# Kernel tuning notes

Hardware: AMD Instinct MI355X
Metric: run time of the kernel (lower is better)

The kernel has to match this reference:

```python
import jax, jax.numpy as jnp
import numpy as np

OUT_H, OUT_W = 14, 14
SPATIAL_SCALE = 0.25

def setup_inputs() -> dict:
    key = jax.random.key(0)
    k1, k2, k3, k4, k5, k6 = jax.random.split(key, 6)
    B, C, H, W = 2, 256, 200, 336
    R = 1000
    features = jax.random.normal(k1, (B, C, H, W), jnp.float32)
    img_h, img_w = H / SPATIAL_SCALE, W / SPATIAL_SCALE
    cx = jax.random.uniform(k2, (R,)) * img_w
    cy = jax.random.uniform(k3, (R,)) * img_h
    bw = jax.random.uniform(k4, (R,)) * 256.0 + 16.0
    bh = jax.random.uniform(k5, (R,)) * 256.0 + 16.0
    x1 = jnp.clip(cx - bw / 2, 0.0, img_w - 1.0)
    x2 = jnp.clip(cx + bw / 2, 0.0, img_w - 1.0)
    y1 = jnp.clip(cy - bh / 2, 0.0, img_h - 1.0)
    y2 = jnp.clip(cy + bh / 2, 0.0, img_h - 1.0)
    bidx = jax.random.randint(k6, (R,), 0, B).astype(jnp.float32)
    rois = jnp.stack([bidx, x1, y1, x2, y2], axis=1)  # (R, 5)
    return {"features": features, "rois": rois}

def _roi_align(features, rois):
    # features: (B, C, H, W); rois: (R, 5) = (batch_idx, x1, y1, x2, y2) in image coords
    B, C, H, W = features.shape
    R = rois.shape[0]
    b = jax.lax.stop_gradient(rois[:, 0]).astype(jnp.int32)
    x1, y1, x2, y2 = rois[:, 1], rois[:, 2], rois[:, 3], rois[:, 4]
    # bin-center grid in [0,1] (affine_grid identity, align_corners=False, then normalized)
    gx = (jnp.arange(OUT_W, dtype=features.dtype) + 0.5) / OUT_W
    gy = (jnp.arange(OUT_H, dtype=features.dtype) + 0.5) / OUT_H
    px = x1[:, None] + gx[None, :] * (x2 - x1)[:, None]  # (R, OUT_W) abs image x
    py = y1[:, None] + gy[None, :] * (y2 - y1)[:, None]  # (R, OUT_H) abs image y
    # grid_sample(align_corners=False) with normalized coord abs/(size/scale): pix = abs*scale - 0.5
    fx = jnp.broadcast_to(px[:, None, :], (R, OUT_H, OUT_W)) * SPATIAL_SCALE - 0.5
    fy = jnp.broadcast_to(py[:, :, None], (R, OUT_H, OUT_W)) * SPATIAL_SCALE - 0.5
    x0 = jnp.floor(fx); y0 = jnp.floor(fy)
    lx = fx - x0; ly = fy - y0
    x0i = x0.astype(jnp.int32); y0i = y0.astype(jnp.int32)
    feats_flat = features.reshape(B, C, H * W)
    bb = b[:, None, None]  # (R,1,1)
    def corner(yi, xi):
        valid = ((xi >= 0) & (xi < W) & (yi >= 0) & (yi < H)).astype(features.dtype)
        idx = jnp.clip(yi, 0, H - 1) * W + jnp.clip(xi, 0, W - 1)  # (R,OUT_H,OUT_W)
        v = feats_flat[bb, :, idx]  # (R, OUT_H, OUT_W, C)
        return v * valid[..., None]  # zeros padding_mode
    v00 = corner(y0i, x0i)
    v01 = corner(y0i, x0i + 1)
    v10 = corner(y0i + 1, x0i)
    v11 = corner(y0i + 1, x0i + 1)
    wx0 = (1.0 - lx)[..., None]; wx1 = lx[..., None]
    wy0 = (1.0 - ly)[..., None]; wy1 = ly[..., None]
    out = wy0 * (wx0 * v00 + wx1 * v01) + wy1 * (wx0 * v10 + wx1 * v11)
    return out.transpose(0, 3, 1, 2)  # (R, C, OUT_H, OUT_W)

def reference(features, rois):
    return _roi_align(features, rois)
```

## Files before the change

### kernel.cpp

```cpp
#include <hip/hip_runtime.h>

constexpr int B = 2, C = 256, H = 200, W = 336;
constexpr int HW = H * W;
constexpr int OH = 14, OW = 14, OHW = OH * OW;
constexpr float SCALE = 0.25f;
constexpr int R = 1000;

constexpr int CSPLIT = 4;
constexpr int CPB = C / CSPLIT;
constexpr int NXCD = 8;
constexpr int RPX = R / NXCD;

typedef float f2 __attribute__((ext_vector_type(2), aligned(4)));

__global__ __launch_bounds__(1024) void sort_rois_kernel(
    const float* __restrict__ rois, int* __restrict__ order)
{
    __shared__ unsigned key[1024];
    const int t = threadIdx.x;

    unsigned k = 0xFFFFFFFFu;
    if (t < R) {
        const float* roi = rois + t * 5;
        const int   b  = (int)roi[0];
        const float cx = 0.5f * (roi[1] + roi[3]);
        const float cy = 0.5f * (roi[2] + roi[4]);
        const int yb   = min(12, max(0, (int)cy >> 6));
        const int band = (b << 4) | yb;
        const int cxi  = min(2047, max(0, (int)cx));
        k = ((unsigned)band << 21) | ((unsigned)cxi << 10) | (unsigned)t;
    }
    key[t] = k;

    for (int size = 2; size <= 1024; size <<= 1) {
        for (int stride = size >> 1; stride > 0; stride >>= 1) {
            __syncthreads();
            const int j = t ^ stride;
            if (j > t) {
                const bool up = ((t & size) == 0);
                const unsigned a = key[t], b2 = key[j];
                if ((a > b2) == up) { key[t] = b2; key[j] = a; }
            }
        }
    }
    __syncthreads();
    if (t < R) order[t] = (int)(key[t] & 1023u);
}

__global__ __launch_bounds__(256) void roi_align_kernel(
    const float* __restrict__ feat,
    const float* __restrict__ rois,
    const int*  __restrict__ order,
    float* __restrict__ out)
{
    const int bid   = blockIdx.x;
    const int xcd   = bid & (NXCD - 1);
    const int slot  = bid >> 3;
    const int slice = slot & (CSPLIT - 1);
    const int rank  = slot >> 2;
    const int r     = order[xcd * RPX + rank];
    const int c0    = slice * CPB;
    const int tid   = threadIdx.x;

    const float* roi = rois + r * 5;
    const float bf = roi[0];
    const float x1 = roi[1], y1 = roi[2], x2 = roi[3], y2 = roi[4];
    const int b = __builtin_amdgcn_readfirstlane((int)bf);

    const int s = tid;
    if (s >= OHW) return;

    const int oh = s / OW;
    const int ow = s - oh * OW;

    const float fx = (x1 + (ow + 0.5f) * (1.0f / OW) * (x2 - x1)) * SCALE - 0.5f;
    const float fy = (y1 + (oh + 0.5f) * (1.0f / OH) * (y2 - y1)) * SCALE - 0.5f;

    const float x0f = floorf(fx), y0f = floorf(fy);
    const float lx = fx - x0f,   ly = fy - y0f;
    const int x0 = (int)x0f,  y0 = (int)y0f;
    const int x1i = x0 + 1,   y1i = y0 + 1;

    const float cxw0 = ((x0  >= 0 && x0  < W) ? 1.0f : 0.0f) * (1.0f - lx);
    const float cxw1 = ((x1i >= 0 && x1i < W) ? 1.0f : 0.0f) * lx;
    const float ryw0 = ((y0  >= 0 && y0  < H) ? 1.0f : 0.0f) * (1.0f - ly);
    const float ryw1 = ((y1i >= 0 && y1i < H) ? 1.0f : 0.0f) * ly;

    const int px = min(max(x0, 0), W - 2);
    const bool swp = (x0 != px);
    const float wxa = swp ? cxw1 : cxw0;
    const float wxb = swp ? cxw0 : cxw1;
    const float a0 = ryw0 * wxa, b0 = ryw0 * wxb;
    const float a1 = ryw1 * wxa, b1 = ryw1 * wxb;

    const int cy0 = min(max(y0,  0), H - 1);
    const int cy1 = min(max(y1i, 0), H - 1);
    const int i0 = cy0 * W + px;
    const int i1 = cy1 * W + px;

    const float* p  = feat + (size_t)(b * C + c0) * HW;
    float*       op = out  + (size_t)r * C * OHW + (size_t)c0 * OHW + s;

    #pragma unroll 8
    for (int c = 0; c < CPB; ++c) {
        const f2 r0 = *reinterpret_cast<const f2*>(p + i0);
        const f2 r1 = *reinterpret_cast<const f2*>(p + i1);
        *op = fmaf(a0, r0.x, fmaf(b0, r0.y, fmaf(a1, r1.x, b1 * r1.y)));
        p  += HW;
        op += OHW;
    }
}

extern "C" void kernel_launch(void* const* d_in, const int* in_sizes, int n_in,
                              void* d_out, int out_size, void* d_ws, size_t ws_size,
                              hipStream_t stream) {
    const float* feat = (const float*)d_in[0];
    const float* rois = (const float*)d_in[1];
    float* out = (float*)d_out;
    int* order = (int*)d_ws;

    sort_rois_kernel<<<1, 1024, 0, stream>>>(rois, order);

    dim3 grid(R * CSPLIT);
    dim3 block(256);
    roi_align_kernel<<<grid, block, 0, stream>>>(feat, rois, order, out);
}
```

Baseline: 413.3 us.

## Bucket ROIs by 2D tile, split channels 16 ways, batch loads, nontemporal stores

Replaces the bitonic sort of ROIs with a counting-sort over batch/y/x tiles of 64 pixels, using shared-memory atomics and a prefix scan. This gives 2D locality instead of row-band ordering, though ROIs within a bucket end up in nondeterministic order. The channel split rises from 4 to 16, so there are four times as many smaller blocks, and launch bounds request higher occupancy. The inner loop now issues 8 channels of gathers before computing, and writes output with nontemporal stores to avoid polluting cache.

After: 387.4 us. -6.3%, faster.

```diff
diff --git a/kernel.cpp b/kernel.cpp
--- a/kernel.cpp
+++ b/kernel.cpp
@@ -6,48 +6,52 @@
 constexpr float SCALE = 0.25f;
 constexpr int R = 1000;
 
-constexpr int CSPLIT = 4;
+constexpr int CSPLIT = 16;
 constexpr int CPB = C / CSPLIT;
 constexpr int NXCD = 8;
 constexpr int RPX = R / NXCD;
 
+constexpr int NYB = 13;
+constexpr int NXB = 21;
+constexpr int NBUCKET = B * NYB * NXB;
+
 typedef float f2 __attribute__((ext_vector_type(2), aligned(4)));
 
-__global__ __launch_bounds__(1024) void sort_rois_kernel(
+__global__ __launch_bounds__(1024) void bucket_rois_kernel(
     const float* __restrict__ rois, int* __restrict__ order)
 {
-    __shared__ unsigned key[1024];
+    __shared__ int cnt[1024];
     const int t = threadIdx.x;
+    cnt[t] = 0;
+    __syncthreads();
 
-    unsigned k = 0xFFFFFFFFu;
+    int k = 0, pos = 0;
     if (t < R) {
         const float* roi = rois + t * 5;
         const int   b  = (int)roi[0];
         const float cx = 0.5f * (roi[1] + roi[3]);
         const float cy = 0.5f * (roi[2] + roi[4]);
-        const int yb   = min(12, max(0, (int)cy >> 6));
-        const int band = (b << 4) | yb;
-        const int cxi  = min(2047, max(0, (int)cx));
-        k = ((unsigned)band << 21) | ((unsigned)cxi << 10) | (unsigned)t;
-    }
-    key[t] = k;
-
-    for (int size = 2; size <= 1024; size <<= 1) {
-        for (int stride = size >> 1; stride > 0; stride >>= 1) {
-            __syncthreads();
-            const int j = t ^ stride;
-            if (j > t) {
-                const bool up = ((t & size) == 0);
-                const unsigned a = key[t], b2 = key[j];
-                if ((a > b2) == up) { key[t] = b2; key[j] = a; }
-            }
-        }
+        const int yb = min(NYB - 1, max(0, (int)cy >> 6));
+        const int xb = min(NXB - 1, max(0, (int)cx >> 6));
+        k = (b * NYB + yb) * NXB + xb;
+        pos = atomicAdd(&cnt[k], 1);
     }
     __syncthreads();
-    if (t < R) order[t] = (int)(key[t] & 1023u);
+
+    for (int off = 1; off < 1024; off <<= 1) {
+        const int add = (t >= off) ? cnt[t - off] : 0;
+        __syncthreads();
+        cnt[t] += add;
+        __syncthreads();
+    }
+
+    if (t < R) {
+        const int base = (k > 0) ? cnt[k - 1] : 0;
+        order[base + pos] = t;
+    }
 }
 
-__global__ __launch_bounds__(256) void roi_align_kernel(
+__global__ __launch_bounds__(256, 8) void roi_align_kernel(
     const float* __restrict__ feat,
     const float* __restrict__ rois,
     const int*  __restrict__ order,
@@ -57,17 +61,16 @@
     const int xcd   = bid & (NXCD - 1);
     const int slot  = bid >> 3;
     const int slice = slot & (CSPLIT - 1);
-    const int rank  = slot >> 2;
-    const int r     = order[xcd * RPX + rank];
+    const int rank  = slot >> 4;
+    const int r     = __builtin_amdgcn_readfirstlane(order[xcd * RPX + rank]);
     const int c0    = slice * CPB;
-    const int tid   = threadIdx.x;
+    const int s     = threadIdx.x;
 
     const float* roi = rois + r * 5;
     const float bf = roi[0];
     const float x1 = roi[1], y1 = roi[2], x2 = roi[3], y2 = roi[4];
     const int b = __builtin_amdgcn_readfirstlane((int)bf);
 
-    const int s = tid;
     if (s >= OHW) return;
 
     const int oh = s / OW;
@@ -101,13 +104,24 @@
     const float* p  = feat + (size_t)(b * C + c0) * HW;
     float*       op = out  + (size_t)r * C * OHW + (size_t)c0 * OHW + s;
 
-    #pragma unroll 8
-    for (int c = 0; c < CPB; ++c) {
-        const f2 r0 = *reinterpret_cast<const f2*>(p + i0);
-        const f2 r1 = *reinterpret_cast<const f2*>(p + i1);
-        *op = fmaf(a0, r0.x, fmaf(b0, r0.y, fmaf(a1, r1.x, b1 * r1.y)));
-        p  += HW;
-        op += OHW;
+    #pragma unroll 1
+    for (int cb = 0; cb < CPB; cb += 8) {
+        f2 v0[8], v1[8];
+        #pragma unroll
+        for (int u = 0; u < 8; ++u) {
+            const float* pc = p + (size_t)u * HW;
+            v0[u] = *reinterpret_cast<const f2*>(pc + i0);
+            v1[u] = *reinterpret_cast<const f2*>(pc + i1);
+        }
+        #pragma unroll
+        for (int u = 0; u < 8; ++u) {
+            const float v = fmaf(a0, v0[u].x,
+                            fmaf(b0, v0[u].y,
+                            fmaf(a1, v1[u].x, b1 * v1[u].y)));
+            __builtin_nontemporal_store(v, op + u * OHW);
+        }
+        p  += (size_t)8 * HW;
+        op += 8 * OHW;
     }
 }
 
@@ -119,7 +133,7 @@
     float* out = (float*)d_out;
     int* order = (int*)d_ws;
 
-    sort_rois_kernel<<<1, 1024, 0, stream>>>(rois, order);
+    bucket_rois_kernel<<<1, 1024, 0, stream>>>(rois, order);
 
     dim3 grid(R * CSPLIT);
     dim3 block(256);
```
